# Kernel optimization log

Hardware: AMD Instinct MI355X
Metric: run time of the kernel (lower is better)

Reference implementation:

```python
import jax, jax.numpy as jnp
import numpy as np

GAMMA = 0.00390625  # 1/256


def setup_inputs() -> dict:
    key = jax.random.key(0)
    ks = jax.random.split(key, 8)
    B, F, S = 65536, 256, 1024
    return {
        "x": jax.random.normal(ks[0], (B, F), dtype=jnp.float32),
        "sv": jax.random.normal(ks[1], (S, F), dtype=jnp.float32),
        "W1": jax.random.normal(ks[2], (S, S), dtype=jnp.float32) * (1.0 / np.sqrt(S)),
        "b1": jax.random.normal(ks[3], (S,), dtype=jnp.float32) * 0.01,
        "W2": jax.random.normal(ks[4], (S, S), dtype=jnp.float32) * (1.0 / np.sqrt(S)),
        "b2": jax.random.normal(ks[5], (S,), dtype=jnp.float32) * 0.01,
        "Wh": jax.random.normal(ks[6], (2, S), dtype=jnp.float32) * (1.0 / np.sqrt(S)),
        "bh": jax.random.normal(ks[7], (2,), dtype=jnp.float32) * 0.01,
    }


def reference(x, sv, W1, b1, W2, b2, Wh, bh):
    # RBF kernel features: k[b, s] = exp(-gamma * ||x_b - sv_s||^2)
    # Expand squared distance to avoid a (B, S, F) intermediate.
    x2 = jnp.sum(x * x, axis=-1, keepdims=True)          # (B, 1)
    s2 = jnp.sum(sv * sv, axis=-1)[None, :]              # (1, S)
    d2 = x2 + s2 - 2.0 * jnp.einsum("bf,sf->bs", x, sv)  # (B, S)
    k = jnp.exp(-GAMMA * d2)                              # (B, S)
    # MLP classifier: depth=2 hidden ReLU layers + 2-logit head
    h = jax.nn.relu(jnp.einsum("bs,os->bo", k, W1) + b1)
    h = jax.nn.relu(jnp.einsum("bs,os->bo", h, W2) + b2)
    return jnp.einsum("bs,os->bo", h, Wh) + bh           # (B, 2)
```

## Files before the change

kernel.cpp:

```cpp
#include <hip/hip_runtime.h>

typedef _Float16 f16x8 __attribute__((ext_vector_type(8)));
typedef _Float16 f16x4 __attribute__((ext_vector_type(4)));
typedef float    f32x4 __attribute__((ext_vector_type(4)));

#define GAMMA_F 0.00390625f

__global__ __launch_bounds__(256) void prep_rows_kernel(
    const float* __restrict__ src, _Float16* __restrict__ dst,
    float* __restrict__ sq, int nrows)
{
    int lane = threadIdx.x & 63, w = threadIdx.x >> 6;
    int row = blockIdx.x * 4 + w;
    if (row >= nrows) return;
    float4 v = ((const float4*)(src + (size_t)row * 256))[lane];
    f16x4 h;
    h[0] = (_Float16)v.x; h[1] = (_Float16)v.y;
    h[2] = (_Float16)v.z; h[3] = (_Float16)v.w;
    *((f16x4*)(dst + (size_t)row * 256) + lane) = h;
    float ss = v.x*v.x + v.y*v.y + v.z*v.z + v.w*v.w;
#pragma unroll
    for (int off = 32; off; off >>= 1) ss += __shfl_down(ss, off);
    if (lane == 0) sq[row] = ss;
}

__global__ __launch_bounds__(256) void cvt_kernel(
    const float* __restrict__ src, _Float16* __restrict__ dst, int n4)
{
    int i = blockIdx.x * 256 + threadIdx.x;
    if (i < n4) {
        float4 v = ((const float4*)src)[i];
        f16x4 h;
        h[0] = (_Float16)v.x; h[1] = (_Float16)v.y;
        h[2] = (_Float16)v.z; h[3] = (_Float16)v.w;
        ((f16x4*)dst)[i] = h;
    }
}

__device__ __forceinline__ void stage_pair(
    const _Float16* __restrict__ A, const _Float16* __restrict__ B,
    int rowA0, int rowB0, int k0, int ld, int t,
    f16x8* Abuf, f16x8* Bbuf)
{
#pragma unroll
    for (int i = 0; i < 4; ++i) {
        int p   = i * 256 + t;
        int row = p >> 3;
        int cg  = (p & 7) ^ (row & 7);
        const _Float16* ga = A + (size_t)(rowA0 + row) * ld + k0 + cg * 8;
        __builtin_amdgcn_global_load_lds(
            (const __attribute__((address_space(1))) void*)ga,
            (__attribute__((address_space(3))) void*)(Abuf + p), 16, 0, 0);
        const _Float16* gb = B + (size_t)(rowB0 + row) * ld + k0 + cg * 8;
        __builtin_amdgcn_global_load_lds(
            (const __attribute__((address_space(1))) void*)gb,
            (__attribute__((address_space(3))) void*)(Bbuf + p), 16, 0, 0);
    }
}

template <int MODE, int K>
__global__ __launch_bounds__(256) void gemm_kernel(
    const _Float16* __restrict__ A, const _Float16* __restrict__ B,
    _Float16* __restrict__ C, const float* __restrict__ e0,
    const float* __restrict__ e1)
{
    constexpr int KT = K / 64;
    __shared__ f16x8 Abuf[1024];
    __shared__ f16x8 Bbuf[1024];

    int t    = threadIdx.x;
    int lane = t & 63, w = t >> 6;
    int wr   = w >> 1, wc = w & 1;
    int lrow = lane & 15, kq = lane >> 4;

    int bid  = blockIdx.x;
    int MBv  = (int)(gridDim.x >> 3);
    int lbid = (bid & 7) * MBv + (bid >> 3);
    int bm   = lbid >> 3, bn = lbid & 7;
    int rowA0 = bm * 128, rowB0 = bn * 128;

    f32x4 acc[4][4];
#pragma unroll
    for (int i = 0; i < 4; ++i)
#pragma unroll
        for (int j = 0; j < 4; ++j) acc[i][j] = (f32x4){0.f, 0.f, 0.f, 0.f};

    stage_pair(A, B, rowA0, rowB0, 0, K, t, Abuf, Bbuf);
    __syncthreads();

    for (int kt = 0; kt < KT; ++kt) {
#pragma unroll
        for (int ks = 0; ks < 2; ++ks) {
            int c   = ks * 4 + kq;
            int swz = c ^ (lrow & 7);
            f16x8 af[4], bf[4];
#pragma unroll
            for (int mi = 0; mi < 4; ++mi)
                af[mi] = Abuf[(wr * 64 + mi * 16 + lrow) * 8 + swz];
#pragma unroll
            for (int ni = 0; ni < 4; ++ni)
                bf[ni] = Bbuf[(wc * 64 + ni * 16 + lrow) * 8 + swz];
#pragma unroll
            for (int mi = 0; mi < 4; ++mi)
#pragma unroll
                for (int ni = 0; ni < 4; ++ni)
                    acc[mi][ni] = __builtin_amdgcn_mfma_f32_16x16x32_f16(
                        af[mi], bf[ni], acc[mi][ni], 0, 0, 0);
        }
        if (kt + 1 < KT) {
            __syncthreads();
            stage_pair(A, B, rowA0, rowB0, (kt + 1) * 64, K, t, Abuf, Bbuf);
            __syncthreads();
        }
    }

    int gr0 = rowA0 + wr * 64;
    int gc0 = rowB0 + wc * 64;
    float ecol[4];
#pragma unroll
    for (int ni = 0; ni < 4; ++ni)
        ecol[ni] = (MODE == 0) ? e1[gc0 + ni * 16 + lrow]
                               : e0[gc0 + ni * 16 + lrow];
#pragma unroll
    for (int mi = 0; mi < 4; ++mi) {
#pragma unroll
        for (int j = 0; j < 4; ++j) {
            int row = gr0 + mi * 16 + kq * 4 + j;
            float xr = (MODE == 0) ? e0[row] : 0.f;
            size_t base = (size_t)row * 1024 + gc0 + lrow;
#pragma unroll
            for (int ni = 0; ni < 4; ++ni) {
                float v = acc[mi][ni][j];
                if (MODE == 0) {
                    v = __expf(-GAMMA_F * (xr + ecol[ni] - 2.f * v));
                } else {
                    v += ecol[ni];
                    v = fmaxf(v, 0.f);
                }
                C[base + (size_t)ni * 16] = (_Float16)v;
            }
        }
    }
}

__global__ __launch_bounds__(256) void head_kernel(
    const _Float16* __restrict__ h2, const float* __restrict__ Wh,
    const float* __restrict__ bh, float* __restrict__ out)
{
    int lane = threadIdx.x & 63, w = threadIdx.x >> 6;
    int row = blockIdx.x * 4 + w;
    const _Float16* hp = h2 + (size_t)row * 1024;
    float s0 = 0.f, s1 = 0.f;
#pragma unroll
    for (int i = 0; i < 2; ++i) {
        int base = (i * 64 + lane) * 8;
        f16x8 hv = *(const f16x8*)(hp + base);
#pragma unroll
        for (int j = 0; j < 8; ++j) {
            float hj = (float)hv[j];
            s0 = fmaf(hj, Wh[base + j], s0);
            s1 = fmaf(hj, Wh[1024 + base + j], s1);
        }
    }
#pragma unroll
    for (int off = 32; off; off >>= 1) {
        s0 += __shfl_down(s0, off);
        s1 += __shfl_down(s1, off);
    }
    if (lane == 0) {
        out[(size_t)row * 2 + 0] = s0 + bh[0];
        out[(size_t)row * 2 + 1] = s1 + bh[1];
    }
}

extern "C" void kernel_launch(void* const* d_in, const int* in_sizes, int n_in,
                              void* d_out, int out_size, void* d_ws, size_t ws_size,
                              hipStream_t stream)
{
    const float* x  = (const float*)d_in[0];
    const float* sv = (const float*)d_in[1];
    const float* W1 = (const float*)d_in[2];
    const float* b1 = (const float*)d_in[3];
    const float* W2 = (const float*)d_in[4];
    const float* b2 = (const float*)d_in[5];
    const float* Wh = (const float*)d_in[6];
    const float* bh = (const float*)d_in[7];
    float* out = (float*)d_out;
    char* ws = (char*)d_ws;

    constexpr size_t OFF_SV = 0;
    constexpr size_t OFF_W1 = OFF_SV + 524288;
    constexpr size_t OFF_W2 = OFF_W1 + 2097152;
    constexpr size_t OFF_S2 = OFF_W2 + 2097152;
    constexpr size_t PERSIST = OFF_S2 + 4096;

    _Float16* svf = (_Float16*)(ws + OFF_SV);
    _Float16* w1f = (_Float16*)(ws + OFF_W1);
    _Float16* w2f = (_Float16*)(ws + OFF_W2);
    float*    s2v = (float*)(ws + OFF_S2);

    int Bc = 65536;
    while (Bc > 128 && PERSIST + (size_t)Bc * 4100ULL > ws_size) Bc >>= 1;

    char* chunk_base = ws + PERSIST;
    _Float16* kb  = (_Float16*)chunk_base;
    _Float16* h1b = (_Float16*)(chunk_base + (size_t)Bc * 2048);
    _Float16* xf  = h1b;
    float*    x2v = (float*)(chunk_base + (size_t)Bc * 4096);

    prep_rows_kernel<<<1024 / 4, 256, 0, stream>>>(sv, svf, s2v, 1024);
    cvt_kernel<<<1024, 256, 0, stream>>>(W1, w1f, 262144);
    cvt_kernel<<<1024, 256, 0, stream>>>(W2, w2f, 262144);

    int nchunks = 65536 / Bc;
    int ggrid   = (Bc / 128) * 8;
    for (int c = 0; c < nchunks; ++c) {
        const float* xc = x + (size_t)c * Bc * 256;
        prep_rows_kernel<<<Bc / 4, 256, 0, stream>>>(xc, xf, x2v, Bc);
        gemm_kernel<0, 256><<<ggrid, 256, 0, stream>>>(xf, svf, kb, x2v, s2v);
        gemm_kernel<1, 1024><<<ggrid, 256, 0, stream>>>(kb, w1f, h1b, b1, nullptr);
        gemm_kernel<1, 1024><<<ggrid, 256, 0, stream>>>(h1b, w2f, kb, b2, nullptr);
        head_kernel<<<Bc / 4, 256, 0, stream>>>(kb, Wh, bh, out + (size_t)c * Bc * 2);
    }
}
```

Baseline: 418.0 us.

## Rewrite GEMM as 256x256-tile, 8-wave double-buffered pipeline with interleaved loads

Replaces the 128x128 single-buffered GEMM with a 256x256 tile computed by 512 threads (8 waves). It double-buffers A and B in LDS (128 KB) and interleaves global-to-LDS loads for upcoming K-tiles between MFMA clusters, using explicit barriers, waitcnt and setprio. The goal is to raise arithmetic intensity and hide global load latency behind MFMAs, instead of stalling on a full sync around every stage. In exchange it uses more registers and LDS per block, relies on hand-tuned vmcnt counts that are fragile, and its grid and column mapping assume N=1024.

Measured after the change: 405.4 us. -3.0%, faster.

```diff
diff --git a/kernel.cpp b/kernel.cpp
--- a/kernel.cpp
+++ b/kernel.cpp
@@ -37,84 +37,142 @@
     }
 }
 
-__device__ __forceinline__ void stage_pair(
-    const _Float16* __restrict__ A, const _Float16* __restrict__ B,
-    int rowA0, int rowB0, int k0, int ld, int t,
-    f16x8* Abuf, f16x8* Bbuf)
-{
-#pragma unroll
-    for (int i = 0; i < 4; ++i) {
-        int p   = i * 256 + t;
-        int row = p >> 3;
-        int cg  = (p & 7) ^ (row & 7);
-        const _Float16* ga = A + (size_t)(rowA0 + row) * ld + k0 + cg * 8;
-        __builtin_amdgcn_global_load_lds(
-            (const __attribute__((address_space(1))) void*)ga,
-            (__attribute__((address_space(3))) void*)(Abuf + p), 16, 0, 0);
-        const _Float16* gb = B + (size_t)(rowB0 + row) * ld + k0 + cg * 8;
-        __builtin_amdgcn_global_load_lds(
-            (const __attribute__((address_space(1))) void*)gb,
-            (__attribute__((address_space(3))) void*)(Bbuf + p), 16, 0, 0);
-    }
-}
+#define SBAR()  __builtin_amdgcn_s_barrier()
+#define LGKM0() do { asm volatile("s_waitcnt lgkmcnt(0)" ::: "memory"); \
+                     __builtin_amdgcn_sched_barrier(0); } while (0)
+
+#define STAGE(gbase, ldsbase, half, kt) do {                                   \
+    const _Float16* _g = (gbase) + (size_t)(half) * (128 * K) + (kt) * 64;     \
+    __builtin_amdgcn_global_load_lds(                                          \
+        (const __attribute__((address_space(1))) void*)_g,                     \
+        (__attribute__((address_space(3))) void*)&lds[(ldsbase) + (half)*1024 + t],       \
+        16, 0, 0);                                                             \
+    __builtin_amdgcn_global_load_lds(                                          \
+        (const __attribute__((address_space(1))) void*)(_g + (size_t)64 * K),  \
+        (__attribute__((address_space(3))) void*)&lds[(ldsbase) + (half)*1024 + 512 + t], \
+        16, 0, 0);                                                             \
+} while (0)
+
+#define READ_A(s, mh) do {                                                     \
+    _Pragma("unroll") for (int ks = 0; ks < 2; ++ks)                           \
+    _Pragma("unroll") for (int mi = 0; mi < 4; ++mi)                           \
+        afr[ks][mi] = lds[(s)*2048 +                                           \
+            (wr*128 + (mh)*64 + mi*16 + lrow)*8 + ((ks*4+kq) ^ (lrow&7))];     \
+} while (0)
+
+#define READ_B(s, nh) do {                                                     \
+    _Pragma("unroll") for (int ks = 0; ks < 2; ++ks)                           \
+    _Pragma("unroll") for (int nb = 0; nb < 2; ++nb)                           \
+        bfr[ks][(nh)*2+nb] = lds[4096 + (s)*2048 +                             \
+            (wc*64 + (nh)*32 + nb*16 + lrow)*8 + ((ks*4+kq) ^ (lrow&7))];      \
+} while (0)
+
+#define MFMA16(mh, nh) do {                                                    \
+    __builtin_amdgcn_s_setprio(1);                                             \
+    _Pragma("unroll") for (int mi = 0; mi < 4; ++mi)                           \
+    _Pragma("unroll") for (int nb = 0; nb < 2; ++nb)                           \
+    _Pragma("unroll") for (int ks = 0; ks < 2; ++ks)                           \
+        acc[(mh)*4+mi][(nh)*2+nb] = __builtin_amdgcn_mfma_f32_16x16x32_f16(    \
+            afr[ks][mi], bfr[ks][(nh)*2+nb], acc[(mh)*4+mi][(nh)*2+nb], 0,0,0);\
+    __builtin_amdgcn_s_setprio(0);                                             \
+} while (0)
 
 template <int MODE, int K>
-__global__ __launch_bounds__(256) void gemm_kernel(
+__global__ __launch_bounds__(512, 2) void gemm256_kernel(
     const _Float16* __restrict__ A, const _Float16* __restrict__ B,
     _Float16* __restrict__ C, const float* __restrict__ e0,
     const float* __restrict__ e1)
 {
     constexpr int KT = K / 64;
-    __shared__ f16x8 Abuf[1024];
-    __shared__ f16x8 Bbuf[1024];
-
-    int t    = threadIdx.x;
-    int lane = t & 63, w = t >> 6;
-    int wr   = w >> 1, wc = w & 1;
-    int lrow = lane & 15, kq = lane >> 4;
+    constexpr int NITER = KT / 2;
+    __shared__ f16x8 lds[8192];
+
+    const int t    = threadIdx.x;
+    const int lane = t & 63, w = t >> 6;
+    const int wr   = w >> 2, wc = w & 3;
+    const int lrow = lane & 15, kq = lane >> 4;
 
     int bid  = blockIdx.x;
-    int MBv  = (int)(gridDim.x >> 3);
-    int lbid = (bid & 7) * MBv + (bid >> 3);
-    int bm   = lbid >> 3, bn = lbid & 7;
-    int rowA0 = bm * 128, rowB0 = bn * 128;
-
-    f32x4 acc[4][4];
-#pragma unroll
-    for (int i = 0; i < 4; ++i)
+    int cpx  = (int)(gridDim.x >> 3);
+    int lbid = (bid & 7) * cpx + (bid >> 3);
+    int bm   = lbid >> 2, bn = lbid & 3;
+    int rowA0 = bm * 256, rowB0 = bn * 256;
+
+    const int prow = t >> 3;
+    const int cg   = (t & 7) ^ (prow & 7);
+    const _Float16* aSB = A + (size_t)(rowA0 + prow) * K + cg * 8;
+    const _Float16* bSB = B + (size_t)(rowB0 + prow) * K + cg * 8;
+
+    f32x4 acc[8][4];
+#pragma unroll
+    for (int i = 0; i < 8; ++i)
 #pragma unroll
         for (int j = 0; j < 4; ++j) acc[i][j] = (f32x4){0.f, 0.f, 0.f, 0.f};
 
-    stage_pair(A, B, rowA0, rowB0, 0, K, t, Abuf, Bbuf);
-    __syncthreads();
-
-    for (int kt = 0; kt < KT; ++kt) {
-#pragma unroll
-        for (int ks = 0; ks < 2; ++ks) {
-            int c   = ks * 4 + kq;
-            int swz = c ^ (lrow & 7);
-            f16x8 af[4], bf[4];
-#pragma unroll
-            for (int mi = 0; mi < 4; ++mi)
-                af[mi] = Abuf[(wr * 64 + mi * 16 + lrow) * 8 + swz];
-#pragma unroll
-            for (int ni = 0; ni < 4; ++ni)
-                bf[ni] = Bbuf[(wc * 64 + ni * 16 + lrow) * 8 + swz];
-#pragma unroll
-            for (int mi = 0; mi < 4; ++mi)
-#pragma unroll
-                for (int ni = 0; ni < 4; ++ni)
-                    acc[mi][ni] = __builtin_amdgcn_mfma_f32_16x16x32_f16(
-                        af[mi], bf[ni], acc[mi][ni], 0, 0, 0);
-        }
-        if (kt + 1 < KT) {
-            __syncthreads();
-            stage_pair(A, B, rowA0, rowB0, (kt + 1) * 64, K, t, Abuf, Bbuf);
-            __syncthreads();
-        }
-    }
-
-    int gr0 = rowA0 + wr * 64;
+    f16x8 afr[2][4], bfr[2][4];
+
+    STAGE(aSB, 0,    0, 0); STAGE(aSB, 0,    1, 0);
+    STAGE(bSB, 4096, 0, 0); STAGE(bSB, 4096, 1, 0);
+    STAGE(aSB, 2048, 0, 1); STAGE(aSB, 2048, 1, 1);
+    STAGE(bSB, 6144, 0, 1); STAGE(bSB, 6144, 1, 1);
+    asm volatile("s_waitcnt vmcnt(8)" ::: "memory");
+    SBAR();
+
+    for (int j = 0; j < NITER; ++j) {
+        const bool last = (j == NITER - 1);
+        const int tA = 2 * j + 1;
+        const int tN = 2 * j + 2;
+        const int tO = 2 * j + 3;
+
+        READ_A(0, 0); READ_B(0, 0);
+        if (j > 0) STAGE(aSB, 2048, 0, tA);
+        SBAR(); LGKM0();
+        MFMA16(0, 0);
+        SBAR();
+        READ_B(0, 1);
+        if (j > 0) STAGE(aSB, 2048, 1, tA);
+        SBAR(); LGKM0();
+        MFMA16(0, 1);
+        SBAR();
+        READ_A(0, 1);
+        if (!last) STAGE(bSB, 4096, 0, tN);
+        SBAR(); LGKM0();
+        MFMA16(1, 0);
+        SBAR();
+        if (!last) {
+            STAGE(bSB, 4096, 1, tN);
+            asm volatile("s_waitcnt vmcnt(4)" ::: "memory");
+        } else {
+            asm volatile("s_waitcnt vmcnt(0)" ::: "memory");
+        }
+        SBAR(); LGKM0();
+        MFMA16(1, 1);
+        SBAR();
+        READ_A(1, 0); READ_B(1, 0);
+        if (!last) STAGE(aSB, 0, 0, tN);
+        SBAR(); LGKM0();
+        MFMA16(0, 0);
+        SBAR();
+        READ_B(1, 1);
+        if (!last) STAGE(aSB, 0, 1, tN);
+        SBAR(); LGKM0();
+        MFMA16(0, 1);
+        SBAR();
+        READ_A(1, 1);
+        if (!last) STAGE(bSB, 6144, 0, tO);
+        SBAR(); LGKM0();
+        MFMA16(1, 0);
+        SBAR();
+        if (!last) {
+            STAGE(bSB, 6144, 1, tO);
+            asm volatile("s_waitcnt vmcnt(4)" ::: "memory");
+        }
+        SBAR(); LGKM0();
+        MFMA16(1, 1);
+        SBAR();
+    }
+
+    int gr0 = rowA0 + wr * 128;
     int gc0 = rowB0 + wc * 64;
     float ecol[4];
 #pragma unroll
@@ -122,15 +180,15 @@
         ecol[ni] = (MODE == 0) ? e1[gc0 + ni * 16 + lrow]
                                : e0[gc0 + ni * 16 + lrow];
 #pragma unroll
-    for (int mi = 0; mi < 4; ++mi) {
-#pragma unroll
-        for (int j = 0; j < 4; ++j) {
-            int row = gr0 + mi * 16 + kq * 4 + j;
+    for (int mi = 0; mi < 8; ++mi) {
+#pragma unroll
+        for (int jj = 0; jj < 4; ++jj) {
+            int row = gr0 + mi * 16 + kq * 4 + jj;
             float xr = (MODE == 0) ? e0[row] : 0.f;
             size_t base = (size_t)row * 1024 + gc0 + lrow;
 #pragma unroll
             for (int ni = 0; ni < 4; ++ni) {
-                float v = acc[mi][ni][j];
+                float v = acc[mi][ni][jj];
                 if (MODE == 0) {
                     v = __expf(-GAMMA_F * (xr + ecol[ni] - 2.f * v));
                 } else {
@@ -200,7 +258,7 @@
     float*    s2v = (float*)(ws + OFF_S2);
 
     int Bc = 65536;
-    while (Bc > 128 && PERSIST + (size_t)Bc * 4100ULL > ws_size) Bc >>= 1;
+    while (Bc > 256 && PERSIST + (size_t)Bc * 4100ULL > ws_size) Bc >>= 1;
 
     char* chunk_base = ws + PERSIST;
     _Float16* kb  = (_Float16*)chunk_base;
@@ -213,13 +271,13 @@
     cvt_kernel<<<1024, 256, 0, stream>>>(W2, w2f, 262144);
 
     int nchunks = 65536 / Bc;
-    int ggrid   = (Bc / 128) * 8;
+    int ggrid   = (Bc / 256) * 4;
     for (int c = 0; c < nchunks; ++c) {
         const float* xc = x + (size_t)c * Bc * 256;
         prep_rows_kernel<<<Bc / 4, 256, 0, stream>>>(xc, xf, x2v, Bc);
-        gemm_kernel<0, 256><<<ggrid, 256, 0, stream>>>(xf, svf, kb, x2v, s2v);
-        gemm_kernel<1, 1024><<<ggrid, 256, 0, stream>>>(kb, w1f, h1b, b1, nullptr);
-        gemm_kernel<1, 1024><<<ggrid, 256, 0, stream>>>(h1b, w2f, kb, b2, nullptr);
+        gemm256_kernel<0, 256><<<ggrid, 512, 0, stream>>>(xf, svf, kb, x2v, s2v);
+        gemm256_kernel<1, 1024><<<ggrid, 512, 0, stream>>>(kb, w1f, h1b, b1, nullptr);
+        gemm256_kernel<1, 1024><<<ggrid, 512, 0, stream>>>(h1b, w2f, kb, b2, nullptr);
         head_kernel<<<Bc / 4, 256, 0, stream>>>(kb, Wh, bh, out + (size_t)c * Bc * 2);
     }
 }
```
